# Kernel tuning notes

Measured on AMD Instinct MI355X. Metric: run time of the kernel, lower is better.

## Reference

```python
import jax, jax.numpy as jnp
import numpy as np

HQ, HK, D = 16, 4, 64
WINDOW = 1024  # sliding-window left size; right=0 (causal)
GATE_CH = 12
RMS_EPS = 1e-8


def rms_norm(x):
    return x * jax.lax.rsqrt(jnp.mean(x * x, axis=-1, keepdims=True) + RMS_EPS)


def apply_rope(x, cos, sin):
    # x: [B,T,H,D]; cos/sin: [T,D//2] broadcast to [1,T,1,D//2]
    x1, x2 = jnp.split(x, 2, axis=-1)
    c = cos[None, :, None, :]
    s = sin[None, :, None, :]
    return jnp.concatenate([x1 * c - x2 * s, x1 * s + x2 * c], axis=-1)


def setup_inputs() -> dict:
    key = jax.random.key(0)
    ks = jax.random.split(key, 7)
    B, T, E = 2, 2048, HQ * D
    x = jax.random.normal(ks[0], (B, T, E), jnp.float32)
    value_embeds = jax.random.normal(ks[1], (B, T, HK * D), jnp.float32)
    # rope cache: angles for half the head dim
    inv_freq = 1.0 / (10000.0 ** (jnp.arange(D // 2, dtype=jnp.float32) / (D // 2)))
    ang = jnp.arange(T, dtype=jnp.float32)[:, None] * inv_freq[None, :]
    rope_cos = jnp.cos(ang)
    rope_sin = jnp.sin(ang)
    std = (3.0 ** 0.5) * (E ** -0.5)
    w_qkv = jax.random.uniform(ks[2], ((HQ + 2 * HK) * D, E), jnp.float32, -std, std)
    w_gate = jax.random.normal(ks[3], (HK, GATE_CH), jnp.float32) * 0.02
    w_o = jax.random.normal(ks[4], (E, E), jnp.float32) * 0.02
    return {"x": x, "value_embeds": value_embeds, "rope_cos": rope_cos,
            "rope_sin": rope_sin, "w_qkv": w_qkv, "w_gate": w_gate, "w_o": w_o}


def reference(x, value_embeds, rope_cos, rope_sin, w_qkv, w_gate, w_o):
    B, T, E = x.shape
    groups = HQ // HK
    qkv = jnp.einsum('bte,fe->btf', x, w_qkv).reshape(B, T, HQ + 2 * HK, D)
    q = qkv[:, :, :HQ, :]
    k = qkv[:, :, HQ:HQ + HK, :]
    v = qkv[:, :, HQ + HK:, :]
    # value-embedding gating
    ve = value_embeds.reshape(B, T, HK, D)
    gate = 3.0 * jax.nn.sigmoid(jnp.einsum('btc,hc->bth', x[..., :GATE_CH], w_gate))
    v = v + gate[..., None] * ve
    # rope + qk-norm
    q = rms_norm(apply_rope(q, rope_cos, rope_sin))
    k = rms_norm(apply_rope(k, rope_cos, rope_sin))
    # GQA: repeat kv heads
    k_rep = jnp.repeat(k, groups, axis=2)  # [B,T,HQ,D]
    v_rep = jnp.repeat(v, groups, axis=2)
    scale = 1.0 / jnp.sqrt(jnp.float32(D))
    scores = jnp.einsum('bqhd,bkhd->bhqk', q, k_rep) * scale
    i = jnp.arange(T)[:, None]
    j = jnp.arange(T)[None, :]
    mask = (j <= i) & (j >= i - WINDOW)  # causal + sliding window
    scores = jnp.where(mask[None, None], scores, jnp.float32(-1e30))
    attn = jax.nn.softmax(scores, axis=-1)
    out = jnp.einsum('bhqk,bkhd->bqhd', attn, v_rep).reshape(B, T, E)
    out = jnp.einsum('bte,fe->btf', out, w_o)
    return out
```

## Files before the change

### kernel.cpp

```cpp
#include <hip/hip_runtime.h>
#include <math.h>

#define T_LEN 2048
#define NB 2
#define E_DIM 1024
#define F_DIM 1536
#define HQn 16
#define HKn 4
#define Dh 64
#define WIN 1024
#define GATE_CH 12
#define PS 72
#define PSV 68
#define CS 73

typedef unsigned short u16;
typedef unsigned int u32;
typedef __attribute__((ext_vector_type(8))) short bf16x8;
typedef __attribute__((ext_vector_type(4))) short bf16x4;
typedef __attribute__((ext_vector_type(4))) float f32x4;

#if __has_builtin(__builtin_amdgcn_mfma_f32_16x16x16bf16_1k)
#define MFMA16(A, B, C) __builtin_amdgcn_mfma_f32_16x16x16bf16_1k(A, B, C, 0, 0, 0)
#elif __has_builtin(__builtin_amdgcn_mfma_f32_16x16x16_bf16)
#define MFMA16(A, B, C) __builtin_amdgcn_mfma_f32_16x16x16_bf16(A, B, C, 0, 0, 0)
#else
static __device__ __forceinline__ f32x4 mfma16_asm(bf16x4 a, bf16x4 b, f32x4 c) {
  f32x4 d;
  asm volatile("s_nop 1\n\tv_mfma_f32_16x16x16_bf16 %0, %1, %2, %3\n\ts_nop 7\n\ts_nop 7"
               : "=v"(d) : "v"(a), "v"(b), "v"(c));
  return d;
}
#define MFMA16(A, B, C) mfma16_asm(A, B, C)
#endif

__device__ __forceinline__ u16 f2bf(float f) {
  union { float f; unsigned int u; } v; v.f = f;
  unsigned int u = v.u + 0x7FFF + ((v.u >> 16) & 1);
  return (u16)(u >> 16);
}
__device__ __forceinline__ float bf2f(u16 h) {
  union { unsigned int u; float f; } v; v.u = ((unsigned int)h) << 16;
  return v.f;
}
__device__ __forceinline__ u32 pack_bf2(float hi, float lo) {
  union { float f; u32 u; } a, b; a.f = hi; b.f = lo;
  return __builtin_amdgcn_perm(a.u + 0x8000u, b.u + 0x8000u, 0x07060302u);
}
__device__ __forceinline__ void async_copy16(const void* g, void* l) {
  __builtin_amdgcn_global_load_lds(
      (const __attribute__((address_space(1))) unsigned int*)g,
      (__attribute__((address_space(3))) unsigned int*)l, 16, 0, 0);
}

__global__ __launch_bounds__(256) void cvt_all(
    const float4* __restrict__ x, const float4* __restrict__ wqkv,
    const float4* __restrict__ wo, uint2* __restrict__ xb,
    uint2* __restrict__ wqb, uint2* __restrict__ wob)
{
  int blk = blockIdx.x;
  const float4* in; uint2* out; int i;
  if (blk < 4096)       { in = x;    out = xb;  i = blk * 256 + threadIdx.x; }
  else if (blk < 5632)  { in = wqkv; out = wqb; i = (blk - 4096) * 256 + threadIdx.x; }
  else                  { in = wo;   out = wob; i = (blk - 5632) * 256 + threadIdx.x; }
  float4 v = in[i];
  uint2 o;
  o.x = (unsigned)f2bf(v.x) | ((unsigned)f2bf(v.y) << 16);
  o.y = (unsigned)f2bf(v.z) | ((unsigned)f2bf(v.w) << 16);
  out[i] = o;
}

__global__ __launch_bounds__(256) void gemm_qkv(
    const u16* __restrict__ A, const u16* __restrict__ B,
    const float* __restrict__ x, const float* __restrict__ ve,
    const float* __restrict__ rcos, const float* __restrict__ rsin,
    const float* __restrict__ wg,
    u16* __restrict__ qa, u16* __restrict__ ka, u16* __restrict__ vt)
{
  constexpr int K = E_DIM;
  constexpr int NT = K / 64;
  __shared__ u16 smem[16384];
  u16* As = smem;
  u16* Bs = smem + 8192;
  u16* Ct = smem;
  float* gateL = (float*)(smem + 4672);
  const int tid = threadIdx.x;
  const int wave = tid >> 6, lane = tid & 63;
  const int quad = lane >> 4, lanelow = lane & 15;
  const int row0 = blockIdx.x * 64;
  const int h    = blockIdx.y;
  const int col0 = h * 64;
  const int wm = (wave >> 1) * 32, wn = (wave & 1) * 32;

  f32x4 acc[2][2];
#pragma unroll
  for (int i = 0; i < 2; ++i)
#pragma unroll
    for (int j = 0; j < 2; ++j) acc[i][j] = (f32x4){0.f, 0.f, 0.f, 0.f};

  auto stage = [&](int buf, int k0) {
#pragma unroll
    for (int s = 0; s < 2; ++s) {
      int slot = s * 256 + tid;
      int r = slot >> 3, g = (slot & 7) ^ (r & 7);
      async_copy16(A + (size_t)(row0 + r) * K + k0 + g * 8,
                   &As[buf * 4096 + slot * 8]);
    }
#pragma unroll
    for (int s = 0; s < 2; ++s) {
      int slot = s * 256 + tid;
      int r = slot >> 3, g = (slot & 7) ^ (r & 7);
      async_copy16(B + (size_t)(col0 + r) * K + k0 + g * 8,
                   &Bs[buf * 4096 + slot * 8]);
    }
  };

  stage(0, 0);
  stage(1, 64);
  int cur = 0;
  for (int t = 0; t < NT; ++t) {
    if (t < NT - 1) asm volatile("s_waitcnt vmcnt(4)" ::: "memory");
    else            asm volatile("s_waitcnt vmcnt(0)" ::: "memory");
    __builtin_amdgcn_s_barrier();
    __builtin_amdgcn_sched_barrier(0);
#pragma unroll
    for (int kk = 0; kk < 2; ++kk) {
      bf16x8 a[2], b[2];
#pragma unroll
      for (int i = 0; i < 2; ++i) {
        int r = wm + i * 16 + lanelow;
        a[i] = *(const bf16x8*)&As[cur * 4096 + r * 64 + (((kk * 4 + quad) ^ (r & 7)) * 8)];
      }
#pragma unroll
      for (int j = 0; j < 2; ++j) {
        int r = wn + j * 16 + lanelow;
        b[j] = *(const bf16x8*)&Bs[cur * 4096 + r * 64 + (((kk * 4 + quad) ^ (r & 7)) * 8)];
      }
      __builtin_amdgcn_s_setprio(1);
#pragma unroll
      for (int i = 0; i < 2; ++i)
#pragma unroll
        for (int j = 0; j < 2; ++j)
          acc[i][j] = __builtin_amdgcn_mfma_f32_16x16x32_bf16(a[i], b[j], acc[i][j], 0, 0, 0);
      __builtin_amdgcn_s_setprio(0);
    }
    __builtin_amdgcn_sched_barrier(0);
    __builtin_amdgcn_s_barrier();
    if (t + 2 < NT) stage(cur, (t + 2) * 64);
    cur ^= 1;
  }

#pragma unroll
  for (int i = 0; i < 2; ++i)
#pragma unroll
    for (int j = 0; j < 2; ++j)
#pragma unroll
      for (int reg = 0; reg < 4; ++reg) {
        int row = wm + i * 16 + quad * 4 + reg;
        int col = wn + j * 16 + lanelow;
        Ct[row * CS + col] = f2bf(acc[i][j][reg]);
      }
  __syncthreads();

  if (h < HQn + HKn) {
    const bool isq = (h < HQn);
    const int half = lane & 31;
    for (int t = wave * 16; t < wave * 16 + 16; ++t) {
      int tok = row0 + t;
      int tt = tok & (T_LEN - 1);
      float c = rcos[tt * 32 + half], s = rsin[tt * 32 + half];
      float x1 = bf2f(Ct[t * CS + half]);
      float x2 = bf2f(Ct[t * CS + half + 32]);
      float y = (lane < 32) ? (x1 * c - x2 * s) : (x1 * s + x2 * c);
      float ss = y * y;
#pragma unroll
      for (int o = 32; o; o >>= 1) ss += __shfl_xor(ss, o, 64);
      float v = y * rsqrtf(ss * (1.f / Dh) + 1e-8f);
      if (isq)
        qa[((size_t)tok * HQn + h) * Dh + lane] = f2bf(v * 0.1803368801f);
      else
        ka[((size_t)tok * HKn + (h - HQn)) * Dh + lane] = f2bf(v);
    }
  } else {
    const int hk = h - (HQn + HKn);
    if (tid < 64) {
      int tok = row0 + tid;
      float g = 0.f;
#pragma unroll
      for (int c = 0; c < GATE_CH; ++c)
        g += x[(size_t)tok * E_DIM + c] * wg[hk * GATE_CH + c];
      gateL[tid] = 3.f / (1.f + __expf(-g));
    }
    __syncthreads();
    for (int t = wave * 16; t < wave * 16 + 16; ++t) {
      int tok = row0 + t;
      float val = bf2f(Ct[t * CS + lane]) +
                  gateL[t] * ve[(size_t)tok * (HKn * Dh) + hk * Dh + lane];
      Ct[t * CS + lane] = f2bf(val);
    }
    __syncthreads();
    int d = tid >> 2, tseg = (tid & 3) * 16;
    int tokbase = row0 + tseg;
    int b = tokbase >> 11;
    int tloc = tokbase & (T_LEN - 1);
    u16 tmp[16];
#pragma unroll
    for (int e = 0; e < 16; ++e) tmp[e] = Ct[(tseg + e) * CS + d];
    u16* dst = vt + ((size_t)(b * HKn + hk) * Dh + d) * T_LEN + tloc;
#pragma unroll
    for (int p = 0; p < 2; ++p)
      *(uint4*)(dst + p * 8) = *(uint4*)&tmp[p * 8];
  }
}

__global__ __launch_bounds__(256) void gemm_wo(
    const u16* __restrict__ A, const u16* __restrict__ B,
    float* __restrict__ C, int N, int K)
{
  const int NT = K / 64;
  __shared__ u16 smem[16384];
  u16* As = smem;
  u16* Bs = smem + 8192;
  const int tid = threadIdx.x;
  const int wave = tid >> 6, lane = tid & 63;
  const int quad = lane >> 4, lanelow = lane & 15;
  const int row0 = blockIdx.x * 64;
  const int col0 = blockIdx.y * 64;
  const int wm = (wave >> 1) * 32, wn = (wave & 1) * 32;

  f32x4 acc[2][2];
#pragma unroll
  for (int i = 0; i < 2; ++i)
#pragma unroll
    for (int j = 0; j < 2; ++j) acc[i][j] = (f32x4){0.f, 0.f, 0.f, 0.f};

  auto stage = [&](int buf, int k0) {
#pragma unroll
    for (int s = 0; s < 2; ++s) {
      int slot = s * 256 + tid;
      int r = slot >> 3, g = (slot & 7) ^ (r & 7);
      async_copy16(A + (size_t)(row0 + r) * K + k0 + g * 8,
                   &As[buf * 4096 + slot * 8]);
    }
#pragma unroll
    for (int s = 0; s < 2; ++s) {
      int slot = s * 256 + tid;
      int r = slot >> 3, g = (slot & 7) ^ (r & 7);
      async_copy16(B + (size_t)(col0 + r) * K + k0 + g * 8,
                   &Bs[buf * 4096 + slot * 8]);
    }
  };

  stage(0, 0);
  stage(1, 64);
  int cur = 0;
  for (int t = 0; t < NT; ++t) {
    if (t < NT - 1) asm volatile("s_waitcnt vmcnt(4)" ::: "memory");
    else            asm volatile("s_waitcnt vmcnt(0)" ::: "memory");
    __builtin_amdgcn_s_barrier();
    __builtin_amdgcn_sched_barrier(0);
#pragma unroll
    for (int kk = 0; kk < 2; ++kk) {
      bf16x8 a[2], b[2];
#pragma unroll
      for (int i = 0; i < 2; ++i) {
        int r = wm + i * 16 + lanelow;
        a[i] = *(const bf16x8*)&As[cur * 4096 + r * 64 + (((kk * 4 + quad) ^ (r & 7)) * 8)];
      }
#pragma unroll
      for (int j = 0; j < 2; ++j) {
        int r = wn + j * 16 + lanelow;
        b[j] = *(const bf16x8*)&Bs[cur * 4096 + r * 64 + (((kk * 4 + quad) ^ (r & 7)) * 8)];
      }
      __builtin_amdgcn_s_setprio(1);
#pragma unroll
      for (int i = 0; i < 2; ++i)
#pragma unroll
        for (int j = 0; j < 2; ++j)
          acc[i][j] = __builtin_amdgcn_mfma_f32_16x16x32_bf16(a[i], b[j], acc[i][j], 0, 0, 0);
      __builtin_amdgcn_s_setprio(0);
    }
    __builtin_amdgcn_sched_barrier(0);
    __builtin_amdgcn_s_barrier();
    if (t + 2 < NT) stage(cur, (t + 2) * 64);
    cur ^= 1;
  }

#pragma unroll
  for (int i = 0; i < 2; ++i)
#pragma unroll
    for (int j = 0; j < 2; ++j) {
      int r = row0 + wm + i * 16 + quad * 4;
      int c = col0 + wn + j * 16 + lanelow;
#pragma unroll
      for (int reg = 0; reg < 4; ++reg)
        C[(size_t)(r + reg) * N + c] = acc[i][j][reg];
    }
}

__global__ __launch_bounds__(256) void attn_mfma(
    const u16* __restrict__ qa, const u16* __restrict__ ka,
    const u16* __restrict__ vt_g, u16* __restrict__ att)
{
  __shared__ u16 Ks[2][64 * PS];
  __shared__ u16 Vt[2][64 * PSV];
  const int bx = blockIdx.x, h = blockIdx.y, b = blockIdx.z;
  const int j5 = bx & 7;
  const int t5 = (bx >> 3) & 3;
  const int tu = (t5 + (h >> 3) + 2 * b) & 3;
  const int qt = (tu == 0) ? j5
               : (tu == 1) ? (15 - j5)
                           : (16 + 2 * j5 + (tu & 1));
  const int hk = h >> 2;
  const int qb = qt * 64;
  const int tid = threadIdx.x;
  const int wave = tid >> 6, lane = tid & 63;
  const int quad = lane >> 4, lanelow = lane & 15;

  bf16x8 aQ[2];
#pragma unroll
  for (int kk = 0; kk < 2; ++kk)
    aQ[kk] = *(const bf16x8*)(qa +
        ((size_t)(b * T_LEN + qb + wave * 16 + lanelow) * HQn + h) * Dh +
        kk * 32 + quad * 8);

  f32x4 O[4];
  float l = 0.f;
#pragma unroll
  for (int dt = 0; dt < 4; ++dt) O[dt] = (f32x4){0.f, 0.f, 0.f, 0.f};

  const int kt0 = (qt >= 16) ? qt - 16 : 0;
  const int kt1 = qt;

  const int sr0 = tid >> 3,         sc0 = (tid & 7) * 8;
  const int sr1 = (tid + 256) >> 3, sc1 = ((tid + 256) & 7) * 8;
  const u16* kg = ka + (size_t)(b * T_LEN) * (HKn * Dh) + hk * Dh;
  const u16* vg = vt_g + (size_t)(b * HKn + hk) * Dh * T_LEN;

  {
    const int kb = kt0 * 64;
    uint4 k0 = *(const uint4*)(kg + (size_t)(kb + sr0) * (HKn * Dh) + sc0);
    uint4 k1 = *(const uint4*)(kg + (size_t)(kb + sr1) * (HKn * Dh) + sc1);
    uint4 v0 = *(const uint4*)(vg + (size_t)sr0 * T_LEN + kb + sc0);
    uint4 v1 = *(const uint4*)(vg + (size_t)sr1 * T_LEN + kb + sc1);
    *(uint4*)&Ks[0][sr0 * PS + sc0] = k0;
    *(uint4*)&Ks[0][sr1 * PS + sc1] = k1;
    *(uint2*)&Vt[0][sr0 * PSV + sc0]     = make_uint2(v0.x, v0.y);
    *(uint2*)&Vt[0][sr0 * PSV + sc0 + 4] = make_uint2(v0.z, v0.w);
    *(uint2*)&Vt[0][sr1 * PSV + sc1]     = make_uint2(v1.x, v1.y);
    *(uint2*)&Vt[0][sr1 * PSV + sc1 + 4] = make_uint2(v1.z, v1.w);
  }

  for (int kt = kt0; kt <= kt1; ++kt) {
    const int buf = (kt - kt0) & 1;
    const int kb = kt * 64;
    uint4 k0, k1, v0, v1;
    const bool more = (kt < kt1);
    if (more) {
      const int nb = kb + 64;
      k0 = *(const uint4*)(kg + (size_t)(nb + sr0) * (HKn * Dh) + sc0);
      k1 = *(const uint4*)(kg + (size_t)(nb + sr1) * (HKn * Dh) + sc1);
      v0 = *(const uint4*)(vg + (size_t)sr0 * T_LEN + nb + sc0);
      v1 = *(const uint4*)(vg + (size_t)sr1 * T_LEN + nb + sc1);
    }
    __builtin_amdgcn_sched_barrier(0);
    asm volatile("s_waitcnt lgkmcnt(0)" ::: "memory");
    __builtin_amdgcn_s_barrier();
    __builtin_amdgcn_sched_barrier(0);

    f32x4 St[4];
#pragma unroll
    for (int jt = 0; jt < 4; ++jt) {
      bf16x8 aK0 = *(const bf16x8*)&Ks[buf][(jt * 16 + lanelow) * PS + quad * 8];
      bf16x8 aK1 = *(const bf16x8*)&Ks[buf][(jt * 16 + lanelow) * PS + 32 + quad * 8];
      f32x4 acc = (f32x4){-12.f, -12.f, -12.f, -12.f};
      acc = __builtin_amdgcn_mfma_f32_16x16x32_bf16(aK0, aQ[0], acc, 0, 0, 0);
      acc = __builtin_amdgcn_mfma_f32_16x16x32_bf16(aK1, aQ[1], acc, 0, 0, 0);
      St[jt] = acc;
    }
    if (kt == kt1) {
#pragma unroll
      for (int jt = 0; jt < 4; ++jt)
#pragma unroll
        for (int rr = 0; rr < 4; ++rr) {
          int ig = qb + wave * 16 + lanelow;
          int jg = kb + jt * 16 + quad * 4 + rr;
          if (jg > ig) St[jt][rr] = -1e30f;
        }
    } else if (kt == kt0 && qt >= 16) {
#pragma unroll
      for (int jt = 0; jt < 4; ++jt)
#pragma unroll
        for (int rr = 0; rr < 4; ++rr) {
          int ig = qb + wave * 16 + lanelow;
          int jg = kb + jt * 16 + quad * 4 + rr;
          if (jg < ig - WIN) St[jt][rr] = -1e30f;
        }
    }
    bf16x4 Pt[4];
#pragma unroll
    for (int jt = 0; jt < 4; ++jt) {
      float p0 = __builtin_amdgcn_exp2f(St[jt][0]);
      float p1 = __builtin_amdgcn_exp2f(St[jt][1]);
      float p2 = __builtin_amdgcn_exp2f(St[jt][2]);
      float p3 = __builtin_amdgcn_exp2f(St[jt][3]);
      l += (p0 + p1) + (p2 + p3);
      union { uint2 u; bf16x4 v; } pu;
      pu.u.x = pack_bf2(p1, p0);
      pu.u.y = pack_bf2(p3, p2);
      Pt[jt] = pu.v;
    }
#pragma unroll
    for (int dt = 0; dt < 4; ++dt)
#pragma unroll
      for (int jt = 0; jt < 4; ++jt) {
        bf16x4 aV = *(const bf16x4*)&Vt[buf][(dt * 16 + lanelow) * PSV + jt * 16 + quad * 4];
        O[dt] = MFMA16(aV, Pt[jt], O[dt]);
      }
    if (more) {
      __builtin_amdgcn_sched_barrier(0);
      asm volatile("s_waitcnt vmcnt(0)" ::: "memory");
      __builtin_amdgcn_sched_barrier(0);
      const int nbuf = buf ^ 1;
      *(uint4*)&Ks[nbuf][sr0 * PS + sc0] = k0;
      *(uint4*)&Ks[nbuf][sr1 * PS + sc1] = k1;
      *(uint2*)&Vt[nbuf][sr0 * PSV + sc0]     = make_uint2(v0.x, v0.y);
      *(uint2*)&Vt[nbuf][sr0 * PSV + sc0 + 4] = make_uint2(v0.z, v0.w);
      *(uint2*)&Vt[nbuf][sr1 * PSV + sc1]     = make_uint2(v1.x, v1.y);
      *(uint2*)&Vt[nbuf][sr1 * PSV + sc1 + 4] = make_uint2(v1.z, v1.w);
    }
  }

  {
    float s = l;
    s += __shfl_xor(s, 16, 64);
    s += __shfl_xor(s, 32, 64);
    float inv = 1.f / s;
    int qg = qb + wave * 16 + lanelow;
    u16* obase = att + (size_t)(b * T_LEN + qg) * E_DIM + h * Dh;
#pragma unroll
    for (int dt = 0; dt < 4; ++dt) {
      bf16x4 ov;
      ov[0] = (short)f2bf(O[dt][0] * inv);
      ov[1] = (short)f2bf(O[dt][1] * inv);
      ov[2] = (short)f2bf(O[dt][2] * inv);
      ov[3] = (short)f2bf(O[dt][3] * inv);
      *(bf16x4*)(obase + dt * 16 + quad * 4) = ov;
    }
  }
}

extern "C" void kernel_launch(void* const* d_in, const int* in_sizes, int n_in,
                              void* d_out, int out_size, void* d_ws, size_t ws_size,
                              hipStream_t stream)
{
  const float* x    = (const float*)d_in[0];
  const float* ve   = (const float*)d_in[1];
  const float* rc   = (const float*)d_in[2];
  const float* rs   = (const float*)d_in[3];
  const float* wqkv = (const float*)d_in[4];
  const float* wg   = (const float*)d_in[5];
  const float* wo   = (const float*)d_in[6];
  float* out = (float*)d_out;

  char* ws = (char*)d_ws;
  u16* x_bf    = (u16*)(ws);
  u16* wqkv_bf = (u16*)(ws + 8388608);
  u16* wo_bf   = (u16*)(ws + 11534336);
  u16* q_att   = (u16*)(ws + 13631488);
  u16* k_att   = (u16*)(ws + 22020096);
  u16* v_t     = (u16*)(ws + 24117248);
  u16* att     = (u16*)(ws + 26214400);

  cvt_all<<<6656, 256, 0, stream>>>((const float4*)x, (const float4*)wqkv,
                                    (const float4*)wo, (uint2*)x_bf,
                                    (uint2*)wqkv_bf, (uint2*)wo_bf);
  gemm_qkv<<<dim3(64, 24), 256, 0, stream>>>(x_bf, wqkv_bf, x, ve, rc, rs, wg,
                                             q_att, k_att, v_t);
  attn_mfma<<<dim3(T_LEN / 64, HQn, NB), 256, 0, stream>>>(q_att, k_att, v_t, att);
  gemm_wo<<<dim3(64, 16), 256, 0, stream>>>(att, wo_bf, out, E_DIM, E_DIM);
}
```

Before: 158.4 us.

## Process two GQA query heads per attention block to share K/V tiles

Each attention workgroup now handles two query heads that map to the same KV head. Every K/V tile loaded into shared memory and every LDS fragment read then feeds twice as many MFMAs. The grid shrinks by half, which cuts redundant K/V global traffic and LDS reads. The cost is higher register pressure from the doubled Q, S, P and O state, and fewer blocks to balance across CUs.

```diff
diff --git a/kernel.cpp b/kernel.cpp
--- a/kernel.cpp
+++ b/kernel.cpp
@@ -304,30 +304,35 @@
 {
   __shared__ u16 Ks[2][64 * PS];
   __shared__ u16 Vt[2][64 * PSV];
-  const int bx = blockIdx.x, h = blockIdx.y, b = blockIdx.z;
+  const int bx = blockIdx.x, hp = blockIdx.y, b = blockIdx.z;
   const int j5 = bx & 7;
   const int t5 = (bx >> 3) & 3;
-  const int tu = (t5 + (h >> 3) + 2 * b) & 3;
+  const int tu = (t5 + (hp >> 2) + 2 * b) & 3;
   const int qt = (tu == 0) ? j5
                : (tu == 1) ? (15 - j5)
                            : (16 + 2 * j5 + (tu & 1));
-  const int hk = h >> 2;
+  const int h0 = hp * 2;
+  const int hk = h0 >> 2;
   const int qb = qt * 64;
   const int tid = threadIdx.x;
   const int wave = tid >> 6, lane = tid & 63;
   const int quad = lane >> 4, lanelow = lane & 15;
 
-  bf16x8 aQ[2];
-#pragma unroll
-  for (int kk = 0; kk < 2; ++kk)
-    aQ[kk] = *(const bf16x8*)(qa +
-        ((size_t)(b * T_LEN + qb + wave * 16 + lanelow) * HQn + h) * Dh +
-        kk * 32 + quad * 8);
-
-  f32x4 O[4];
-  float l = 0.f;
-#pragma unroll
-  for (int dt = 0; dt < 4; ++dt) O[dt] = (f32x4){0.f, 0.f, 0.f, 0.f};
+  bf16x8 aQ[2][2];
+#pragma unroll
+  for (int s = 0; s < 2; ++s)
+#pragma unroll
+    for (int kk = 0; kk < 2; ++kk)
+      aQ[s][kk] = *(const bf16x8*)(qa +
+          ((size_t)(b * T_LEN + qb + wave * 16 + lanelow) * HQn + h0 + s) * Dh +
+          kk * 32 + quad * 8);
+
+  f32x4 O[2][4];
+  float l[2] = {0.f, 0.f};
+#pragma unroll
+  for (int s = 0; s < 2; ++s)
+#pragma unroll
+    for (int dt = 0; dt < 4; ++dt) O[s][dt] = (f32x4){0.f, 0.f, 0.f, 0.f};
 
   const int kt0 = (qt >= 16) ? qt - 16 : 0;
   const int kt1 = qt;
@@ -368,15 +373,18 @@
     __builtin_amdgcn_s_barrier();
     __builtin_amdgcn_sched_barrier(0);
 
-    f32x4 St[4];
+    f32x4 St[2][4];
 #pragma unroll
     for (int jt = 0; jt < 4; ++jt) {
       bf16x8 aK0 = *(const bf16x8*)&Ks[buf][(jt * 16 + lanelow) * PS + quad * 8];
       bf16x8 aK1 = *(const bf16x8*)&Ks[buf][(jt * 16 + lanelow) * PS + 32 + quad * 8];
-      f32x4 acc = (f32x4){-12.f, -12.f, -12.f, -12.f};
-      acc = __builtin_amdgcn_mfma_f32_16x16x32_bf16(aK0, aQ[0], acc, 0, 0, 0);
-      acc = __builtin_amdgcn_mfma_f32_16x16x32_bf16(aK1, aQ[1], acc, 0, 0, 0);
-      St[jt] = acc;
+#pragma unroll
+      for (int s = 0; s < 2; ++s) {
+        f32x4 acc = (f32x4){-12.f, -12.f, -12.f, -12.f};
+        acc = __builtin_amdgcn_mfma_f32_16x16x32_bf16(aK0, aQ[s][0], acc, 0, 0, 0);
+        acc = __builtin_amdgcn_mfma_f32_16x16x32_bf16(aK1, aQ[s][1], acc, 0, 0, 0);
+        St[s][jt] = acc;
+      }
     }
     if (kt == kt1) {
 #pragma unroll
@@ -385,7 +393,7 @@
         for (int rr = 0; rr < 4; ++rr) {
           int ig = qb + wave * 16 + lanelow;
           int jg = kb + jt * 16 + quad * 4 + rr;
-          if (jg > ig) St[jt][rr] = -1e30f;
+          if (jg > ig) { St[0][jt][rr] = -1e30f; St[1][jt][rr] = -1e30f; }
         }
     } else if (kt == kt0 && qt >= 16) {
 #pragma unroll
@@ -394,28 +402,31 @@
         for (int rr = 0; rr < 4; ++rr) {
           int ig = qb + wave * 16 + lanelow;
           int jg = kb + jt * 16 + quad * 4 + rr;
-          if (jg < ig - WIN) St[jt][rr] = -1e30f;
+          if (jg < ig - WIN) { St[0][jt][rr] = -1e30f; St[1][jt][rr] = -1e30f; }
         }
     }
-    bf16x4 Pt[4];
-#pragma unroll
-    for (int jt = 0; jt < 4; ++jt) {
-      float p0 = __builtin_amdgcn_exp2f(St[jt][0]);
-      float p1 = __builtin_amdgcn_exp2f(St[jt][1]);
-      float p2 = __builtin_amdgcn_exp2f(St[jt][2]);
-      float p3 = __builtin_amdgcn_exp2f(St[jt][3]);
-      l += (p0 + p1) + (p2 + p3);
-      union { uint2 u; bf16x4 v; } pu;
-      pu.u.x = pack_bf2(p1, p0);
-      pu.u.y = pack_bf2(p3, p2);
-      Pt[jt] = pu.v;
-    }
+    bf16x4 Pt[2][4];
+#pragma unroll
+    for (int s = 0; s < 2; ++s)
+#pragma unroll
+      for (int jt = 0; jt < 4; ++jt) {
+        float p0 = __builtin_amdgcn_exp2f(St[s][jt][0]);
+        float p1 = __builtin_amdgcn_exp2f(St[s][jt][1]);
+        float p2 = __builtin_amdgcn_exp2f(St[s][jt][2]);
+        float p3 = __builtin_amdgcn_exp2f(St[s][jt][3]);
+        l[s] += (p0 + p1) + (p2 + p3);
+        union { uint2 u; bf16x4 v; } pu;
+        pu.u.x = pack_bf2(p1, p0);
+        pu.u.y = pack_bf2(p3, p2);
+        Pt[s][jt] = pu.v;
+      }
 #pragma unroll
     for (int dt = 0; dt < 4; ++dt)
 #pragma unroll
       for (int jt = 0; jt < 4; ++jt) {
         bf16x4 aV = *(const bf16x4*)&Vt[buf][(dt * 16 + lanelow) * PSV + jt * 16 + quad * 4];
-        O[dt] = MFMA16(aV, Pt[jt], O[dt]);
+        O[0][dt] = MFMA16(aV, Pt[0][jt], O[0][dt]);
+        O[1][dt] = MFMA16(aV, Pt[1][jt], O[1][dt]);
       }
     if (more) {
       __builtin_amdgcn_sched_barrier(0);
@@ -431,20 +442,21 @@
     }
   }
 
-  {
-    float s = l;
-    s += __shfl_xor(s, 16, 64);
-    s += __shfl_xor(s, 32, 64);
-    float inv = 1.f / s;
+#pragma unroll
+  for (int s = 0; s < 2; ++s) {
+    float sum = l[s];
+    sum += __shfl_xor(sum, 16, 64);
+    sum += __shfl_xor(sum, 32, 64);
+    float inv = 1.f / sum;
     int qg = qb + wave * 16 + lanelow;
-    u16* obase = att + (size_t)(b * T_LEN + qg) * E_DIM + h * Dh;
+    u16* obase = att + (size_t)(b * T_LEN + qg) * E_DIM + (h0 + s) * Dh;
 #pragma unroll
     for (int dt = 0; dt < 4; ++dt) {
       bf16x4 ov;
-      ov[0] = (short)f2bf(O[dt][0] * inv);
-      ov[1] = (short)f2bf(O[dt][1] * inv);
-      ov[2] = (short)f2bf(O[dt][2] * inv);
-      ov[3] = (short)f2bf(O[dt][3] * inv);
+      ov[0] = (short)f2bf(O[s][dt][0] * inv);
+      ov[1] = (short)f2bf(O[s][dt][1] * inv);
+      ov[2] = (short)f2bf(O[s][dt][2] * inv);
+      ov[3] = (short)f2bf(O[s][dt][3] * inv);
       *(bf16x4*)(obase + dt * 16 + quad * 4) = ov;
     }
   }
@@ -477,6 +489,6 @@
                                     (uint2*)wqkv_bf, (uint2*)wo_bf);
   gemm_qkv<<<dim3(64, 24), 256, 0, stream>>>(x_bf, wqkv_bf, x, ve, rc, rs, wg,
                                              q_att, k_att, v_t);
-  attn_mfma<<<dim3(T_LEN / 64, HQn, NB), 256, 0, stream>>>(q_att, k_att, v_t, att);
+  attn_mfma<<<dim3(T_LEN / 64, HQn / 2, NB), 256, 0, stream>>>(q_att, k_att, v_t, att);
   gemm_wo<<<dim3(64, 16), 256, 0, stream>>>(att, wo_bf, out, E_DIM, E_DIM);
 }
```

New measurement: 157.6 us, median of 2. Within noise of the previous version (-0.6%).
